# Kernel tuning notes

Measured on AMD Instinct MI355X. Metric: run time of the kernel, lower is better.

The kernel has to match this reference:

```python
import jax, jax.numpy as jnp
import numpy as np

B, D, K = 16384, 32, 128  # batch, cluster_dim, num_clusters


def setup_inputs() -> dict:
    key = jax.random.key(0)
    x = jax.random.normal(key, (B, D, K), dtype=jnp.float32)
    mu_0 = jnp.zeros((D, K), dtype=jnp.float32)                      # running mean buffer
    L_0 = jnp.broadcast_to(jnp.eye(D, dtype=jnp.float32), (K, D, D)) # running Cholesky buffer
    n_0 = jnp.ones((1,), dtype=jnp.float32)                          # running count
    return {"x": x, "mu_0": mu_0, "L_0": L_0, "n_0": n_0}


def reference(x, mu_0, L_0, n_0):
    # Training-mode forward of ClusterNorm1dv2.
    Bn = x.shape[0]
    eps_eye = jnp.eye(x.shape[1], dtype=x.dtype)
    n0 = n_0[0]
    x_mu = jnp.mean(x, axis=0)                         # [D, K]
    x_cnt = jnp.transpose(x - x_mu[None], (2, 1, 0))   # [K, D, B]
    C = jnp.einsum('kdb,keb->kde', x_cnt, x_cnt)       # [K, D, D] per-cluster scatter
    denom = n0 + Bn
    new_mu = (n0 * mu_0 + Bn * x_mu) / denom           # [D, K]
    x_d = jnp.transpose((x_mu - mu_0)[None], (2, 1, 0))  # [K, D, 1]
    new_cov = (jnp.einsum('kde,kfe->kdf', L_0, L_0) * (n0 / denom)
               + C / denom
               + jnp.einsum('kdo,keo->kde', x_d, x_d) * (n0 * Bn / denom ** 2))
    L = jnp.linalg.cholesky(new_cov + eps_eye)         # [K, D, D]
    xc = jnp.transpose(x - new_mu[None], (2, 1, 0))    # [K, D, B]
    Z = jax.scipy.linalg.solve_triangular(L, xc, lower=True)  # whitening solve
    return jnp.transpose(Z, (2, 1, 0))                 # [B, D, K]
```

## Files before the change

### kernel.cpp

```cpp
#include <hip/hip_runtime.h>
#include <hip/hip_bf16.h>

typedef __attribute__((ext_vector_type(4))) float f32x4;
typedef __attribute__((ext_vector_type(4))) unsigned u32x4;
typedef __attribute__((ext_vector_type(8))) short short8;

#define NB 16384
#define ND 32
#define NK 128

__device__ __forceinline__ unsigned pk2(float lo, float hi){
  float2 f; f.x = lo; f.y = hi;
  __hip_bfloat162 h = __float22bfloat162_rn(f);
  union { __hip_bfloat162 h; unsigned u; } v; v.h = h;
  return v.u;
}

__global__ __launch_bounds__(512, 2) void k1_scatter(const float* __restrict__ x,
                                                     float* __restrict__ part) {
  __shared__ float vs[16384];
  __shared__ float ssr[2048];
  const int t = threadIdx.x;
  const int bx = blockIdx.x;
  const int ktile = bx & 3;
  const int cb = bx >> 2;
  const int k0 = ktile*32;

  const int shalf = t >> 8;
  const int d     = (t >> 3) & 31;
  const int kq    = t & 7;
  const float* xb = x + (size_t)d*128 + k0 + 4*kq;

  const int l = t & 63;
  const int w = t >> 6;

  f32x4 acc[4][4];
  #pragma unroll
  for (int c=0;c<4;c++)
    #pragma unroll
    for (int q=0;q<4;q++){ acc[c][q][0]=0.f; acc[c][q][1]=0.f; acc[c][q][2]=0.f; acc[c][q][3]=0.f; }
  float ssum[4] = {0.f,0.f,0.f,0.f};

  unsigned* vsw = (unsigned*)vs;
  f32x4 La[8], Lb[8];

  {
    const int sb = cb*256 + shalf*16;
    #pragma unroll
    for (int p = 0; p < 8; ++p) {
      const float* src = xb + (size_t)(sb + 2*p)*4096;
      La[p] = *(const f32x4*)src;
      Lb[p] = *(const f32x4*)(src + 4096);
    }
  }

  #pragma unroll
  for (int ch = 0; ch < 8; ++ch) {
    #pragma unroll
    for (int i = 0; i < 4; ++i) {
      unsigned w8[8];
      #pragma unroll
      for (int p = 0; p < 8; ++p) {
        w8[p] = pk2(La[p][i], Lb[p][i]);
        ssum[i] += La[p][i] + Lb[p][i];
      }
      const int c = (kq + i) & 3;
      const int o = (shalf*8 + 4*c) & 15;
      unsigned* rowp = vsw + (4*kq + i)*512 + d*16;
      u32x4 lo4 = { w8[0], w8[1], w8[2], w8[3] };
      u32x4 hi4 = { w8[4], w8[5], w8[6], w8[7] };
      *(u32x4*)(rowp + o)            = lo4;
      *(u32x4*)(rowp + ((o+4)&15))   = hi4;
    }
    __syncthreads();
    if (ch < 7) {
      const int sb = cb*256 + (ch+1)*32 + shalf*16;
      #pragma unroll
      for (int p = 0; p < 8; ++p) {
        const float* src = xb + (size_t)(sb + 2*p)*4096;
        La[p] = *(const f32x4*)src;
        Lb[p] = *(const f32x4*)(src + 4096);
      }
    }
    #pragma unroll
    for (int c = 0; c < 4; ++c) {
      const int kk = w*4 + c;
      const float* base = vs + kk*512;
      const int sg = 4*(((l>>4) + w + c) & 3);
      const short8 f0 = *(const short8*)(base + (l&15)*16       + sg);
      const short8 f1 = *(const short8*)(base + (l&15)*16 + 256 + sg);
      acc[c][0] = __builtin_amdgcn_mfma_f32_16x16x32_bf16(f0, f0, acc[c][0], 0,0,0);
      acc[c][1] = __builtin_amdgcn_mfma_f32_16x16x32_bf16(f0, f1, acc[c][1], 0,0,0);
      acc[c][2] = __builtin_amdgcn_mfma_f32_16x16x32_bf16(f1, f0, acc[c][2], 0,0,0);
      acc[c][3] = __builtin_amdgcn_mfma_f32_16x16x32_bf16(f1, f1, acc[c][3], 0,0,0);
    }
    __syncthreads();
  }

  const int col = l & 15, rw = (l >> 4) * 4;
  #pragma unroll
  for (int c = 0; c < 4; ++c) {
    const int kg = k0 + w*4 + c;
    float* pb = part + ((size_t)cb*128 + kg)*1056;
    #pragma unroll
    for (int i = 0; i < 2; ++i)
      #pragma unroll
      for (int j = 0; j < 2; ++j)
        #pragma unroll
        for (int r = 0; r < 4; ++r)
          pb[(i*16 + rw + r)*32 + j*16 + col] = acc[c][i*2+j][r];
  }
  #pragma unroll
  for (int i = 0; i < 4; ++i)
    ssr[shalf*1024 + d*32 + 4*kq + i] = ssum[i];
  __syncthreads();
  for (int ii = t; ii < 1024; ii += 512) {
    const int dd = ii >> 5, kk2 = ii & 31;
    part[((size_t)cb*128 + k0 + kk2)*1056 + 1024 + dd] = ssr[ii] + ssr[1024 + ii];
  }
}

__global__ void k2a_reduce(const float* __restrict__ part, float* __restrict__ sfin) {
  const size_t idx = (size_t)blockIdx.x*256 + threadIdx.x;
  const float* p = part + idx;
  float a0=0.f,a1=0.f,a2=0.f,a3=0.f;
  for (int c = 0; c < 64; c += 4) {
    a0 += p[(size_t)(c+0)*135168];
    a1 += p[(size_t)(c+1)*135168];
    a2 += p[(size_t)(c+2)*135168];
    a3 += p[(size_t)(c+3)*135168];
  }
  sfin[idx] = (a0+a1)+(a2+a3);
}

__global__ void k2b_chol(const float* __restrict__ sfin,
                         const float* __restrict__ mu0,
                         const float* __restrict__ L0,
                         const float* __restrict__ n0p,
                         float* __restrict__ lpad,
                         float* __restrict__ nmu) {
  const int k = blockIdx.x;
  const int t = threadIdx.x;
  __shared__ float L0s[32*33];
  __shared__ float Am[32*33];
  __shared__ float xdl[32];
  __shared__ float dinv[32];
  const float n0 = n0p[0];
  const float denom = n0 + (float)NB;
  const float* sk = sfin + (size_t)k*1056;

  for (int idx = t; idx < 1024; idx += 256)
    L0s[(idx>>5)*33 + (idx&31)] = L0[k*1024 + idx];
  if (t < 32) {
    const float S  = sk[1024 + t];
    const float m0 = mu0[t*128 + k];
    nmu[t*128 + k] = (n0*m0 + S) / denom;
    xdl[t] = S*(1.0f/NB) - m0;
  }
  __syncthreads();

  const float c1 = n0/denom, c2 = 1.0f/denom;
  const float c3 = n0*(float)NB/(denom*denom);
  for (int idx = t; idx < 1024; idx += 256) {
    const int d = idx>>5, e = idx&31;
    const float M  = sk[d*32 + e];
    const float Sd = sk[1024 + d];
    const float Se = sk[1024 + e];
    const float C = M - Sd*Se*(1.0f/NB);
    float g = 0.f;
    #pragma unroll 8
    for (int f=0; f<32; f++) g += L0s[d*33+f]*L0s[e*33+f];
    float a = g*c1 + C*c2 + xdl[d]*xdl[e]*c3;
    if (d==e) a += 1.0f;
    Am[d*33+e] = a;
  }
  __syncthreads();

  for (int j=0;j<32;j++){
    float acc = 0.f;
    if (t < 32 && t >= j) {
      acc = Am[t*33+j];
      for (int e=0;e<j;e++) acc -= Am[t*33+e]*Am[j*33+e];
    }
    __syncthreads();
    if (t == j) {
      const float dj = sqrtf(acc);
      Am[j*33+j] = dj;
      dinv[j] = 1.0f/dj;
    }
    __syncthreads();
    if (t < 32 && t > j) Am[t*33+j] = acc*dinv[j];
    __syncthreads();
  }

  if (t < 32) {
    const int d = t;
    int rs = 0;
    for (int e=0;e<d;e++) rs += (e+3)>>2;
    rs *= 4;
    const int rl = ((d+3)>>2)*4;
    float* lp = lpad + k*576;
    for (int e=0;e<rl;e++) lp[rs+e] = (e<d) ? Am[d*33+e] : 0.f;
    lp[544+d] = dinv[d];
  }
}

__global__ __launch_bounds__(256, 2) void k3_whiten(const float* __restrict__ x,
                                                    const float* __restrict__ lpad,
                                                    const float* __restrict__ nmu,
                                                    float* __restrict__ out) {
  __shared__ float Lw[32*580];
  __shared__ float muL[32*32];
  const int t = threadIdx.x;
  const int bx = blockIdx.x;
  const int m = (bx >> 3) & 1;
  const int u = ((bx >> 4) << 3) | (bx & 7);
  const int ktile = ((u & 1) << 1) | m;
  const int chunk = u >> 1;
  const int k0 = ktile*32;

  {
    const f32x4* src = (const f32x4*)(lpad + (size_t)k0*576);
    #pragma unroll
    for (int q=0;q<18;q++){
      const int idx = t + q*256;
      const int row = idx/144, col = idx - row*144;
      *(f32x4*)(&Lw[row*580 + col*4]) = src[idx];
    }
    #pragma unroll
    for (int idx=t; idx<1024; idx+=256)
      muL[idx] = nmu[(idx>>5)*128 + k0 + (idx&31)];
  }
  __syncthreads();

  const int kl = t & 31;
  const int so = t >> 5;
  const float* Lrow = &Lw[kl*580];
  const int b0 = chunk*128;

  for (int it=0; it<4; ++it) {
    const int base = b0 + it*32 + so;
    const float* xa = x + (size_t)(base     )*4096 + k0 + kl;
    const float* xb = x + (size_t)(base +  8)*4096 + k0 + kl;
    const float* xc = x + (size_t)(base + 16)*4096 + k0 + kl;
    const float* xd = x + (size_t)(base + 24)*4096 + k0 + kl;
    float vA[32], vB[32], vC[32], vD[32];
    #pragma unroll
    for (int d=0; d<32; ++d) vA[d] = xa[d*128];
    #pragma unroll
    for (int d=0; d<32; ++d) vB[d] = xb[d*128];
    #pragma unroll
    for (int d=0; d<32; ++d) vC[d] = xc[d*128];
    #pragma unroll
    for (int d=0; d<32; ++d) vD[d] = xd[d*128];
    #pragma unroll
    for (int d=0; d<32; ++d) {
      const float m2 = muL[d*32 + kl];
      vA[d] -= m2; vB[d] -= m2; vC[d] -= m2; vD[d] -= m2;
    }
    int rs = 0;
    #pragma unroll
    for (int d=0; d<32; ++d) {
      float sA = vA[d], sB = vB[d], sC = vC[d], sD = vD[d];
      const int nq = (d+3)>>2;
      #pragma unroll
      for (int q=0; q<nq; ++q) {
        const f32x4 Lq = *(const f32x4*)(Lrow + rs + 4*q);
        sA -= Lq[0]*vA[4*q+0] + Lq[1]*vA[4*q+1] + Lq[2]*vA[4*q+2] + Lq[3]*vA[4*q+3];
        sB -= Lq[0]*vB[4*q+0] + Lq[1]*vB[4*q+1] + Lq[2]*vB[4*q+2] + Lq[3]*vB[4*q+3];
        sC -= Lq[0]*vC[4*q+0] + Lq[1]*vC[4*q+1] + Lq[2]*vC[4*q+2] + Lq[3]*vC[4*q+3];
        sD -= Lq[0]*vD[4*q+0] + Lq[1]*vD[4*q+1] + Lq[2]*vD[4*q+2] + Lq[3]*vD[4*q+3];
      }
      const float di = Lrow[544+d];
      vA[d] = sA*di; vB[d] = sB*di; vC[d] = sC*di; vD[d] = sD*di;
      rs += 4*nq;
    }
    float* oa = out + (size_t)(base     )*4096 + k0 + kl;
    float* ob = out + (size_t)(base +  8)*4096 + k0 + kl;
    float* oc = out + (size_t)(base + 16)*4096 + k0 + kl;
    float* od = out + (size_t)(base + 24)*4096 + k0 + kl;
    #pragma unroll
    for (int d=0; d<32; ++d) __builtin_nontemporal_store(vA[d], oa + d*128);
    #pragma unroll
    for (int d=0; d<32; ++d) __builtin_nontemporal_store(vB[d], ob + d*128);
    #pragma unroll
    for (int d=0; d<32; ++d) __builtin_nontemporal_store(vC[d], oc + d*128);
    #pragma unroll
    for (int d=0; d<32; ++d) __builtin_nontemporal_store(vD[d], od + d*128);
  }
}

extern "C" void kernel_launch(void* const* d_in, const int* in_sizes, int n_in,
                              void* d_out, int out_size, void* d_ws, size_t ws_size,
                              hipStream_t stream) {
  const float* x   = (const float*)d_in[0];
  const float* mu0 = (const float*)d_in[1];
  const float* L0  = (const float*)d_in[2];
  const float* n0  = (const float*)d_in[3];
  float* out  = (float*)d_out;
  float* part = out;
  float* sfin = out + 8650752;
  float* lpad = (float*)d_ws;
  float* nmu  = lpad + 128*576;

  k1_scatter<<<256, 512, 0, stream>>>(x, part);
  k2a_reduce<<<528, 256, 0, stream>>>(part, sfin);
  k2b_chol  <<<128, 256, 0, stream>>>(sfin, mu0, L0, n0, lpad, nmu);
  k3_whiten <<<512, 256, 0, stream>>>(x, lpad, nmu, out);
}
```

Baseline: 195.1 us.

## Split scatter kernel into twice as many blocks with smaller batch chunks

```diff
diff --git a/kernel.cpp b/kernel.cpp
--- a/kernel.cpp
+++ b/kernel.cpp
@@ -16,14 +16,15 @@
   return v.u;
 }
 
-__global__ __launch_bounds__(512, 2) void k1_scatter(const float* __restrict__ x,
+__global__ __launch_bounds__(512, 4) void k1_scatter(const float* __restrict__ x,
                                                      float* __restrict__ part) {
   __shared__ float vs[16384];
-  __shared__ float ssr[2048];
   const int t = threadIdx.x;
   const int bx = blockIdx.x;
-  const int ktile = bx & 3;
-  const int cb = bx >> 2;
+  const int m  = (bx >> 3) & 1;
+  const int u  = ((bx >> 4) << 3) | (bx & 7);
+  const int ktile = ((u & 1) << 1) | m;
+  const int cb    = u >> 1;
   const int k0 = ktile*32;
 
   const int shalf = t >> 8;
@@ -42,46 +43,34 @@
   float ssum[4] = {0.f,0.f,0.f,0.f};
 
   unsigned* vsw = (unsigned*)vs;
-  f32x4 La[8], Lb[8];
-
-  {
-    const int sb = cb*256 + shalf*16;
-    #pragma unroll
-    for (int p = 0; p < 8; ++p) {
-      const float* src = xb + (size_t)(sb + 2*p)*4096;
-      La[p] = *(const f32x4*)src;
-      Lb[p] = *(const f32x4*)(src + 4096);
-    }
-  }
-
-  #pragma unroll
-  for (int ch = 0; ch < 8; ++ch) {
-    #pragma unroll
-    for (int i = 0; i < 4; ++i) {
-      unsigned w8[8];
-      #pragma unroll
-      for (int p = 0; p < 8; ++p) {
-        w8[p] = pk2(La[p][i], Lb[p][i]);
-        ssum[i] += La[p][i] + Lb[p][i];
-      }
-      const int c = (kq + i) & 3;
-      const int o = (shalf*8 + 4*c) & 15;
-      unsigned* rowp = vsw + (4*kq + i)*512 + d*16;
-      u32x4 lo4 = { w8[0], w8[1], w8[2], w8[3] };
-      u32x4 hi4 = { w8[4], w8[5], w8[6], w8[7] };
-      *(u32x4*)(rowp + o)            = lo4;
-      *(u32x4*)(rowp + ((o+4)&15))   = hi4;
-    }
-    __syncthreads();
-    if (ch < 7) {
-      const int sb = cb*256 + (ch+1)*32 + shalf*16;
-      #pragma unroll
-      for (int p = 0; p < 8; ++p) {
-        const float* src = xb + (size_t)(sb + 2*p)*4096;
+
+  for (int ch = 0; ch < 4; ++ch) {
+    const int sb = cb*128 + ch*32 + shalf*16;
+    #pragma unroll
+    for (int h = 0; h < 2; ++h) {
+      f32x4 La[4], Lb[4];
+      #pragma unroll
+      for (int p = 0; p < 4; ++p) {
+        const float* src = xb + (size_t)(sb + 2*(4*h + p))*4096;
         La[p] = *(const f32x4*)src;
         Lb[p] = *(const f32x4*)(src + 4096);
       }
-    }
+      #pragma unroll
+      for (int i = 0; i < 4; ++i) {
+        unsigned w4[4];
+        #pragma unroll
+        for (int p = 0; p < 4; ++p) {
+          w4[p] = pk2(La[p][i], Lb[p][i]);
+          ssum[i] += La[p][i] + Lb[p][i];
+        }
+        const int c = (kq + i) & 3;
+        const int o = (shalf*8 + 4*h + 4*c) & 15;
+        unsigned* rowp = vsw + (4*kq + i)*512 + d*16;
+        u32x4 q4 = { w4[0], w4[1], w4[2], w4[3] };
+        *(u32x4*)(rowp + o) = q4;
+      }
+    }
+    __syncthreads();
     #pragma unroll
     for (int c = 0; c < 4; ++c) {
       const int kk = w*4 + c;
@@ -112,11 +101,11 @@
   }
   #pragma unroll
   for (int i = 0; i < 4; ++i)
-    ssr[shalf*1024 + d*32 + 4*kq + i] = ssum[i];
+    vs[shalf*1024 + d*32 + 4*kq + i] = ssum[i];
   __syncthreads();
   for (int ii = t; ii < 1024; ii += 512) {
     const int dd = ii >> 5, kk2 = ii & 31;
-    part[((size_t)cb*128 + k0 + kk2)*1056 + 1024 + dd] = ssr[ii] + ssr[1024 + ii];
+    part[((size_t)cb*128 + k0 + kk2)*1056 + 1024 + dd] = vs[ii] + vs[1024 + ii];
   }
 }
 
@@ -124,7 +113,7 @@
   const size_t idx = (size_t)blockIdx.x*256 + threadIdx.x;
   const float* p = part + idx;
   float a0=0.f,a1=0.f,a2=0.f,a3=0.f;
-  for (int c = 0; c < 64; c += 4) {
+  for (int c = 0; c < 128; c += 4) {
     a0 += p[(size_t)(c+0)*135168];
     a1 += p[(size_t)(c+1)*135168];
     a2 += p[(size_t)(c+2)*135168];
@@ -299,11 +288,11 @@
   const float* n0  = (const float*)d_in[3];
   float* out  = (float*)d_out;
   float* part = out;
-  float* sfin = out + 8650752;
+  float* sfin = out + 17301504;
   float* lpad = (float*)d_ws;
   float* nmu  = lpad + 128*576;
 
-  k1_scatter<<<256, 512, 0, stream>>>(x, part);
+  k1_scatter<<<512, 512, 0, stream>>>(x, part);
   k2a_reduce<<<528, 256, 0, stream>>>(part, sfin);
   k2b_chol  <<<128, 256, 0, stream>>>(sfin, mu0, L0, n0, lpad, nmu);
   k3_whiten <<<512, 256, 0, stream>>>(x, lpad, nmu, out);
```

Measured after the change: 297.8 us. +52.7%, slower.
